# Kernel optimization log

Measured on AMD Instinct MI355X. Metric: run time of the kernel, lower is better.

The kernel has to match this reference:

```python
import jax, jax.numpy as jnp
import numpy as np

D_MODEL = 1024
D_FF = 4096
NUM_EXPERTS = 8
TOP_K = 2
BATCH = 2
SEQ = 2048


def setup_inputs() -> dict:
    key = jax.random.key(0)
    ks = jax.random.split(key, 6)
    s_in = 1.0 / np.sqrt(D_MODEL)
    s_ff = 1.0 / np.sqrt(D_FF)
    return {
        "x": jax.random.normal(ks[0], (BATCH, SEQ, D_MODEL), dtype=jnp.float32),
        "gate_w": jax.random.normal(ks[1], (D_MODEL, NUM_EXPERTS), dtype=jnp.float32) * s_in,
        "w1": jax.random.normal(ks[2], (NUM_EXPERTS, D_MODEL, D_FF), dtype=jnp.float32) * s_in,
        "b1": jnp.zeros((NUM_EXPERTS, D_FF), dtype=jnp.float32),
        "w2": jax.random.normal(ks[3], (NUM_EXPERTS, D_FF, D_MODEL), dtype=jnp.float32) * s_ff,
        "b2": jnp.zeros((NUM_EXPERTS, D_MODEL), dtype=jnp.float32),
    }


def reference(x, gate_w, w1, b1, w2, b2):
    B, S, D = x.shape
    T = B * S
    # Router: logits -> softmax -> top-k -> renormalize selected weights
    router_logits = jnp.einsum("bsd,de->bse", x, gate_w)  # [B,S,E]
    probs = jax.nn.softmax(router_logits, axis=-1)
    top_k_weights, top_k_indices = jax.lax.top_k(probs, TOP_K)  # [B,S,K]
    top_k_weights = top_k_weights / jnp.sum(top_k_weights, axis=-1, keepdims=True)

    x_flat = x.reshape(T, D)
    # per-token, per-expert combine weight: sum over k of weight * (idx==e) -> [T,E]
    one_hot = jax.nn.one_hot(top_k_indices.reshape(T, TOP_K), NUM_EXPERTS, dtype=x.dtype)
    combine = jnp.einsum("tke,tk->te", one_hot, top_k_weights.reshape(T, TOP_K))

    # Dense grouped-GEMM over all experts (same math as masked gather/scatter loop,
    # since combine weight is zero for unselected experts)
    h = jnp.maximum(jnp.einsum("td,edf->etf", x_flat, w1) + b1[:, None, :], 0.0)  # [E,T,F]
    y = jnp.einsum("etf,efd->etd", h, w2) + b2[:, None, :]  # [E,T,D]
    out_flat = jnp.einsum("etd,te->td", y, combine)  # [T,D]
    output = out_flat.reshape(B, S, D)
    return output, router_logits, top_k_indices, top_k_weights
```

## Files before the change

kernel.cpp:

```cpp
#include <hip/hip_runtime.h>
#include <cstdint>
#include <cstddef>


#define D_MODEL 1024
#define D_FF    4096
#define NEXP    8
#define TOKENS  4096
#define SLOTS   8192
#define SLOTSP  9216

typedef __bf16 bf16x8 __attribute__((ext_vector_type(8)));
typedef float  f32x4  __attribute__((ext_vector_type(4)));

static __device__ __forceinline__ unsigned short f2bf(float f) {
  unsigned int u = __float_as_uint(f);
  u += 0x7fffu + ((u >> 16) & 1u);
  return (unsigned short)(u >> 16);
}

static __device__ __forceinline__ void async_ld16(const void* g, void* l) {
  __builtin_amdgcn_global_load_lds(
      (const __attribute__((address_space(1))) void*)g,
      (__attribute__((address_space(3))) void*)l, 16, 0, 0);
}


__global__ void init_kernel(int* __restrict__ tok_list) {
  const int g = blockIdx.x * 256 + threadIdx.x;
  if (g < SLOTSP) tok_list[g] = -1;
}

__global__ __launch_bounds__(256) void router_kernel(
    const float* __restrict__ x, const float* __restrict__ gw,
    float* __restrict__ out_logits, float* __restrict__ out_idx,
    float* __restrict__ out_w)
{
  const int w = threadIdx.x >> 6, lane = threadIdx.x & 63;
  const int t = blockIdx.x * 4 + w;
  float p[NEXP];
#pragma unroll
  for (int e = 0; e < NEXP; ++e) p[e] = 0.f;
  const float* xr = x + (size_t)t * D_MODEL;
#pragma unroll 4
  for (int i = 0; i < D_MODEL / 64; ++i) {
    const int d = i * 64 + lane;
    const float xv = xr[d];
    const float* g = gw + (size_t)d * NEXP;
#pragma unroll
    for (int e = 0; e < NEXP; ++e) p[e] += xv * g[e];
  }
#pragma unroll
  for (int e = 0; e < NEXP; ++e) {
#pragma unroll
    for (int s = 1; s < 64; s <<= 1) p[e] += __shfl_xor(p[e], s, 64);
  }
  if (lane == 0) {
    int i0 = 0;
#pragma unroll
    for (int e = 1; e < NEXP; ++e) if (p[e] > p[i0]) i0 = e;
    int i1 = (i0 == 0) ? 1 : 0;
#pragma unroll
    for (int e = 0; e < NEXP; ++e)
      if (e != i0 && p[e] > p[i1]) i1 = e;
    const float w0 = 1.f / (1.f + __expf(p[i1] - p[i0]));
#pragma unroll
    for (int e = 0; e < NEXP; ++e) out_logits[(size_t)t * NEXP + e] = p[e];
    out_idx[t * 2 + 0] = (float)i0;
    out_idx[t * 2 + 1] = (float)i1;
    out_w[t * 2 + 0] = w0;
    out_w[t * 2 + 1] = 1.f - w0;
  }
}

__global__ __launch_bounds__(256) void count_offsets_kernel(
    const float* __restrict__ out_idx, int* __restrict__ wsI)
{
  __shared__ int hist[NEXP];
  const int tid = threadIdx.x;
  if (tid < NEXP) hist[tid] = 0;
  if (tid < NEXP) wsI[8 + tid] = 0;
  __syncthreads();
  int c[NEXP];
#pragma unroll
  for (int e = 0; e < NEXP; ++e) c[e] = 0;
  for (int p = tid * 32; p < tid * 32 + 32; ++p) c[(int)out_idx[p]]++;
#pragma unroll
  for (int e = 0; e < NEXP; ++e) if (c[e]) atomicAdd(&hist[e], c[e]);
  __syncthreads();
  if (tid == 0) {
    int s = 0, nb = 0;
    for (int e = 0; e < NEXP; ++e) {
      wsI[16 + e] = s;
      const int nblk = (hist[e] + 127) >> 7;
      for (int j = 0; j < nblk; ++j) {
        wsI[32 + nb] = e;
        wsI[128 + nb] = s + j * 128;
        ++nb;
      }
      s += nblk << 7;
    }
    wsI[16 + NEXP] = s;
    wsI[25] = nb;
  }
}

__global__ void scatter_kernel(const float* __restrict__ out_idx,
                               int* __restrict__ cursor,
                               const int* __restrict__ po,
                               int* __restrict__ pair_slot,
                               int* __restrict__ tok_list)
{
  const int p = blockIdx.x * 256 + threadIdx.x;
  const int lane = threadIdx.x & 63;
  const int e = (int)out_idx[p];
  int pos = 0;
#pragma unroll
  for (int e8 = 0; e8 < NEXP; ++e8) {
    const unsigned long long m = __ballot(e == e8);
    if (m) {
      const int leader = __ffsll((long long)m) - 1;
      int base = 0;
      if (lane == leader) base = atomicAdd(&cursor[e8], (int)__popcll(m));
      base = __shfl(base, leader, 64);
      if (e == e8)
        pos = po[e8] + base +
              (int)__popcll(m & ((1ull << lane) - 1ull));
    }
  }
  tok_list[pos] = p >> 1;
  pair_slot[p] = pos;
}

__global__ __launch_bounds__(256) void gather_cvt(
    const float* __restrict__ x, const int* __restrict__ tok_list,
    unsigned short* __restrict__ xg)
{
  const int gid = blockIdx.x * 256 + threadIdx.x;
  const int row = gid >> 7, seg = gid & 127;
  const int tok = tok_list[row];
  if (tok < 0) return;
  const float* src = x + (size_t)tok * D_MODEL + seg * 8;
  const float4 a = *(const float4*)(src);
  const float4 b = *(const float4*)(src + 4);
  ushort4 lo = make_ushort4(f2bf(a.x), f2bf(a.y), f2bf(a.z), f2bf(a.w));
  ushort4 hi = make_ushort4(f2bf(b.x), f2bf(b.y), f2bf(b.z), f2bf(b.w));
  unsigned short* d = xg + (size_t)row * D_MODEL + seg * 8;
  *(ushort4*)(d) = lo;
  *(ushort4*)(d + 4) = hi;
}

__global__ __launch_bounds__(256) void transpose_cvt(
    const float* __restrict__ src, unsigned short* __restrict__ dst,
    int K, int N)
{
  const int e = blockIdx.z;
  const int n0 = blockIdx.x * 64;
  const int k0 = blockIdx.y * 64;
  __shared__ float t[64][65];
  const int c4 = (threadIdx.x & 15) * 4;
  const int r  = threadIdx.x >> 4;
  const float* s = src + (size_t)e * K * N + (size_t)k0 * N + n0;
#pragma unroll
  for (int i = 0; i < 4; ++i) {
    const float4 v = *(const float4*)(s + (size_t)(r + 16 * i) * N + c4);
    t[r + 16 * i][c4 + 0] = v.x;
    t[r + 16 * i][c4 + 1] = v.y;
    t[r + 16 * i][c4 + 2] = v.z;
    t[r + 16 * i][c4 + 3] = v.w;
  }
  __syncthreads();
  unsigned short* d = dst + (size_t)e * N * K + (size_t)n0 * K + k0;
#pragma unroll
  for (int i = 0; i < 4; ++i) {
    const int n = r + 16 * i;
    ushort4 v;
    v.x = f2bf(t[c4 + 0][n]);
    v.y = f2bf(t[c4 + 1][n]);
    v.z = f2bf(t[c4 + 2][n]);
    v.w = f2bf(t[c4 + 3][n]);
    *(ushort4*)(d + (size_t)n * K + c4) = v;
  }
}

template <int RELU>
__global__ __launch_bounds__(256) void gemm_mfma(
    const unsigned short* __restrict__ A, const unsigned short* __restrict__ Bt,
    const float* __restrict__ bias, void* __restrict__ Cout,
    const int* __restrict__ wsI, int K, int N)
{
  if ((int)blockIdx.y >= wsI[25]) return;
  const int e = wsI[32 + blockIdx.y];
  const int gr0 = wsI[128 + blockIdx.y];
  const int col0 = blockIdx.x * 128;

  __shared__ unsigned short ldsA[128 * 64];
  __shared__ unsigned short ldsB[128 * 64];

  const int tid = threadIdx.x;
  const int lane = tid & 63;
  const int w = tid >> 6;
  const int wr = w >> 1, wc = w & 1;
  const int m15 = lane & 15, q = lane >> 4;

  f32x4 zero = {0.f, 0.f, 0.f, 0.f};
  f32x4 acc[4][4];
#pragma unroll
  for (int mt = 0; mt < 4; ++mt)
#pragma unroll
    for (int nt = 0; nt < 4; ++nt) acc[mt][nt] = zero;

  const size_t off0 = (size_t)(tid >> 3) * K + ((tid & 7) ^ ((tid >> 3) & 7)) * 8;
  const size_t jstep = (size_t)32 * K;
  const unsigned short* Abase = A + (size_t)gr0 * K;
  const unsigned short* Bbase = Bt + (size_t)e * N * K + (size_t)col0 * K;

  const int sw = q ^ (m15 & 7);

  for (int kk = 0; kk < K; kk += 64) {
#pragma unroll
    for (int j = 0; j < 4; ++j)
      async_ld16(Abase + off0 + j * jstep + kk, &ldsA[(j * 256 + tid) * 8]);
#pragma unroll
    for (int j = 0; j < 4; ++j)
      async_ld16(Bbase + off0 + j * jstep + kk, &ldsB[(j * 256 + tid) * 8]);
    __syncthreads();
#pragma unroll
    for (int ks2 = 0; ks2 < 2; ++ks2) {
      const int slot8 = (sw ^ (ks2 << 2)) * 8;
      bf16x8 af[4], bf[4];
#pragma unroll
      for (int mt = 0; mt < 4; ++mt)
        af[mt] = *(const bf16x8*)&ldsA[(wr * 64 + mt * 16 + m15) * 64 + slot8];
#pragma unroll
      for (int nt = 0; nt < 4; ++nt)
        bf[nt] = *(const bf16x8*)&ldsB[(wc * 64 + nt * 16 + m15) * 64 + slot8];
#pragma unroll
      for (int mt = 0; mt < 4; ++mt)
#pragma unroll
        for (int nt = 0; nt < 4; ++nt)
          acc[mt][nt] = __builtin_amdgcn_mfma_f32_16x16x32_bf16(
              af[mt], bf[nt], acc[mt][nt], 0, 0, 0);
    }
    __syncthreads();
  }

#pragma unroll
  for (int nt = 0; nt < 4; ++nt) {
    const int c = col0 + wc * 64 + nt * 16 + m15;
    const float bv = bias[(size_t)e * N + c];
#pragma unroll
    for (int mt = 0; mt < 4; ++mt) {
      const size_t rbase = (size_t)(gr0 + wr * 64 + mt * 16 + q * 4);
      if (RELU) {
        unsigned short* Cp = (unsigned short*)Cout;
#pragma unroll
        for (int i = 0; i < 4; ++i)
          Cp[(rbase + i) * N + c] = f2bf(fmaxf(acc[mt][nt][i] + bv, 0.f));
      } else {
        float* Cp = (float*)Cout;
#pragma unroll
        for (int i = 0; i < 4; ++i)
          Cp[(rbase + i) * N + c] = acc[mt][nt][i] + bv;
      }
    }
  }
}

__global__ __launch_bounds__(256) void combine_kernel(
    const float* __restrict__ y, const int* __restrict__ pair_slot,
    const float* __restrict__ out_w, float* __restrict__ out)
{
  const int gid = blockIdx.x * 256 + threadIdx.x;
  if (gid >= TOKENS * (D_MODEL / 4)) return;
  const int t = gid >> 8;
  const int qd = gid & 255;
  const float w0 = out_w[t * 2 + 0], w1 = out_w[t * 2 + 1];
  const int p0 = pair_slot[t * 2 + 0], p1 = pair_slot[t * 2 + 1];
  const float4 a = *(const float4*)(y + (size_t)p0 * D_MODEL + qd * 4);
  const float4 b = *(const float4*)(y + (size_t)p1 * D_MODEL + qd * 4);
  float4 o;
  o.x = w0 * a.x + w1 * b.x;
  o.y = w0 * a.y + w1 * b.y;
  o.z = w0 * a.z + w1 * b.z;
  o.w = w0 * a.w + w1 * b.w;
  *(float4*)(out + (size_t)t * D_MODEL + qd * 4) = o;
}

extern "C" void kernel_launch(void* const* d_in, const int* in_sizes, int n_in,
                              void* d_out, int out_size, void* d_ws, size_t ws_size,
                              hipStream_t stream)
{
  (void)in_sizes; (void)n_in; (void)out_size; (void)ws_size;
  const float* x  = (const float*)d_in[0];
  const float* gw = (const float*)d_in[1];
  const float* w1 = (const float*)d_in[2];
  const float* b1 = (const float*)d_in[3];
  const float* w2 = (const float*)d_in[4];
  const float* b2 = (const float*)d_in[5];

  float* out        = (float*)d_out;
  float* out_logits = out + (size_t)TOKENS * D_MODEL;
  float* out_idx    = out_logits + (size_t)TOKENS * NEXP;
  float* out_w      = out_idx + (size_t)TOKENS * 2;

  int* wsI       = (int*)d_ws;
  int* po        = wsI + 16;
  int* tok_list  = wsI + 512;
  int* pair_slot = wsI + 10240;
  unsigned short* xg  = (unsigned short*)((char*)d_ws + (1 << 17));
  unsigned short* w1t = xg  + (size_t)SLOTSP * D_MODEL;
  unsigned short* w2t = w1t + (size_t)NEXP * D_FF * D_MODEL;
  unsigned short* h   = w2t + (size_t)NEXP * D_MODEL * D_FF;
  float*          y   = (float*)(h + (size_t)SLOTSP * D_FF);

  init_kernel<<<SLOTSP / 256, 256, 0, stream>>>(tok_list);
  router_kernel<<<TOKENS / 4, 256, 0, stream>>>(x, gw, out_logits, out_idx, out_w);
  count_offsets_kernel<<<1, 256, 0, stream>>>(out_idx, wsI);
  scatter_kernel<<<SLOTS / 256, 256, 0, stream>>>(out_idx, wsI + 8, po, pair_slot, tok_list);
  gather_cvt<<<SLOTSP * 128 / 256, 256, 0, stream>>>(x, tok_list, xg);
  transpose_cvt<<<dim3(D_FF / 64, D_MODEL / 64, NEXP), 256, 0, stream>>>(w1, w1t, D_MODEL, D_FF);
  transpose_cvt<<<dim3(D_MODEL / 64, D_FF / 64, NEXP), 256, 0, stream>>>(w2, w2t, D_FF, D_MODEL);
  gemm_mfma<1><<<dim3(D_FF / 128, 72, 1), 256, 0, stream>>>(
      xg, w1t, b1, (void*)h, wsI, D_MODEL, D_FF);
  gemm_mfma<0><<<dim3(D_MODEL / 128, 72, 1), 256, 0, stream>>>(
      h, w2t, b2, (void*)y, wsI, D_FF, D_MODEL);
  combine_kernel<<<(TOKENS * D_MODEL / 4) / 256, 256, 0, stream>>>(
      y, pair_slot, out_w, out);
}
```

Baseline: 659.4 us.

## Double-buffer LDS tiles, remap workgroups across XCDs, raise MFMA priority

The expert GEMM now uses two LDS buffers, so the next K-tile's async global-to-LDS loads are issued before the MFMAs on the current tile run, overlapping memory latency with compute. Workgroup IDs are permuted so that consecutive tiles land on the same XCD, which should improve L2 reuse of shared weight and activation tiles. MFMA blocks are wrapped in s_setprio to favour the math waves. LDS use doubles to 64KB per block, which may reduce occupancy. The remap assumes the total workgroup count divides by 8.

```diff
diff --git a/kernel.cpp b/kernel.cpp
--- a/kernel.cpp
+++ b/kernel.cpp
@@ -189,13 +189,21 @@
     const float* __restrict__ bias, void* __restrict__ Cout,
     const int* __restrict__ wsI, int K, int N)
 {
-  if ((int)blockIdx.y >= wsI[25]) return;
-  const int e = wsI[32 + blockIdx.y];
-  const int gr0 = wsI[128 + blockIdx.y];
-  const int col0 = blockIdx.x * 128;
-
-  __shared__ unsigned short ldsA[128 * 64];
-  __shared__ unsigned short ldsB[128 * 64];
+  const int gx = gridDim.x;
+  const int nwg = gx * gridDim.y;
+  const int cpx = nwg >> 3;
+  int f = blockIdx.y * gx + blockIdx.x;
+  f = (f & 7) * cpx + (f >> 3);
+  const int bx = f % gx;
+  const int by = f / gx;
+
+  if (by >= wsI[25]) return;
+  const int e   = wsI[32 + by];
+  const int gr0 = wsI[128 + by];
+  const int col0 = bx * 128;
+
+  __shared__ unsigned short ldsA[2][128 * 64];
+  __shared__ unsigned short ldsB[2][128 * 64];
 
   const int tid = threadIdx.x;
   const int lane = tid & 63;
@@ -217,32 +225,41 @@
 
   const int sw = q ^ (m15 & 7);
 
+  auto stage = [&](int buf, int kk) {
+#pragma unroll
+    for (int j = 0; j < 4; ++j) {
+      async_ld16(Abase + off0 + j * jstep + kk, &ldsA[buf][(j * 256 + tid) * 8]);
+      async_ld16(Bbase + off0 + j * jstep + kk, &ldsB[buf][(j * 256 + tid) * 8]);
+    }
+  };
+
+  stage(0, 0);
+  __syncthreads();
+
+  int cur = 0;
   for (int kk = 0; kk < K; kk += 64) {
-#pragma unroll
-    for (int j = 0; j < 4; ++j)
-      async_ld16(Abase + off0 + j * jstep + kk, &ldsA[(j * 256 + tid) * 8]);
-#pragma unroll
-    for (int j = 0; j < 4; ++j)
-      async_ld16(Bbase + off0 + j * jstep + kk, &ldsB[(j * 256 + tid) * 8]);
-    __syncthreads();
+    if (kk + 64 < K) stage(cur ^ 1, kk + 64);
 #pragma unroll
     for (int ks2 = 0; ks2 < 2; ++ks2) {
       const int slot8 = (sw ^ (ks2 << 2)) * 8;
       bf16x8 af[4], bf[4];
 #pragma unroll
       for (int mt = 0; mt < 4; ++mt)
-        af[mt] = *(const bf16x8*)&ldsA[(wr * 64 + mt * 16 + m15) * 64 + slot8];
+        af[mt] = *(const bf16x8*)&ldsA[cur][(wr * 64 + mt * 16 + m15) * 64 + slot8];
 #pragma unroll
       for (int nt = 0; nt < 4; ++nt)
-        bf[nt] = *(const bf16x8*)&ldsB[(wc * 64 + nt * 16 + m15) * 64 + slot8];
+        bf[nt] = *(const bf16x8*)&ldsB[cur][(wc * 64 + nt * 16 + m15) * 64 + slot8];
+      __builtin_amdgcn_s_setprio(1);
 #pragma unroll
       for (int mt = 0; mt < 4; ++mt)
 #pragma unroll
         for (int nt = 0; nt < 4; ++nt)
           acc[mt][nt] = __builtin_amdgcn_mfma_f32_16x16x32_bf16(
               af[mt], bf[nt], acc[mt][nt], 0, 0, 0);
+      __builtin_amdgcn_s_setprio(0);
     }
     __syncthreads();
+    cur ^= 1;
   }
 
 #pragma unroll
```

Result: no change. 655.5 us (-0.6%).
